# Kernel optimization log

Measured on AMD Instinct MI355X. Metric: run time of the kernel, lower is better.

The kernel has to match this reference:

```python
import jax, jax.numpy as jnp
import numpy as np

EPS = 1e-5
K = 20

def _bn(x, g, b, m, v, caxis):
    shape = [1] * x.ndim
    shape[caxis] = x.shape[caxis]
    rs = lambda p: p.reshape(shape)
    return (x - rs(m)) * (rs(g) / jnp.sqrt(rs(v) + EPS)) + rs(b)

def _lrelu(x):
    return jnp.where(x > 0, x, 0.2 * x)

def _graph_feature(x, k):
    # x: [B, C, N] -> [B, N, k, 2C]
    xt = jnp.swapaxes(x, 1, 2)                       # [B, N, C]
    xx = jnp.sum(x * x, axis=1)                      # [B, N]
    dist = xx[:, :, None] + xx[:, None, :] - 2.0 * jnp.einsum('bnc,bmc->bnm', xt, xt)
    _, idx = jax.lax.top_k(-dist, k)                 # smallest distances, [B, N, k]
    nbr = jax.vmap(lambda t, i: t[i])(xt, idx)       # [B, N, k, C]
    center = xt[:, :, None, :]
    return jnp.concatenate([jnp.broadcast_to(center, nbr.shape), nbr - center], axis=-1)

def _edgeconv(x, W, g, b, m, v, k):
    feat = _graph_feature(x, k)                      # [B, N, k, 2C]
    y = jnp.einsum('bnkc,oc->bonk', feat, W)         # 1x1 conv2d
    y = _lrelu(_bn(y, g, b, m, v, caxis=1))
    return jnp.max(y, axis=-1)                       # [B, O, N]


def setup_inputs() -> dict:
    key = jax.random.key(0)
    ks = jax.random.split(key, 40)
    d = {}
    d['x'] = jax.random.normal(ks[0], (8, 3, 2048), dtype=jnp.float32)
    def mk_w(k_, o, i):
        return jax.random.normal(k_, (o, i), dtype=jnp.float32) * (1.0 / np.sqrt(i))
    def mk_bn(k_, c, pfx, out):
        k1, k2, k3, k4 = jax.random.split(k_, 4)
        out[pfx + '_g'] = jax.random.normal(k1, (c,), jnp.float32) * 0.1 + 1.0
        out[pfx + '_b'] = jax.random.normal(k2, (c,), jnp.float32) * 0.1
        out[pfx + '_m'] = jax.random.normal(k3, (c,), jnp.float32) * 0.1
        out[pfx + '_v'] = jax.random.uniform(k4, (c,), jnp.float32) + 0.5
    d['W1'] = mk_w(ks[1], 64, 6);    mk_bn(ks[2], 64, 'bn1', d)
    d['W2'] = mk_w(ks[3], 64, 128);  mk_bn(ks[4], 64, 'bn2', d)
    d['W3'] = mk_w(ks[5], 128, 128); mk_bn(ks[6], 128, 'bn3', d)
    d['W4'] = mk_w(ks[7], 256, 256); mk_bn(ks[8], 256, 'bn4', d)
    d['W5'] = mk_w(ks[9], 1024, 512); mk_bn(ks[10], 1024, 'bn5', d)
    d['L1'] = mk_w(ks[11], 512, 2048); mk_bn(ks[12], 512, 'bn6', d)
    d['L2'] = mk_w(ks[13], 256, 512);  mk_bn(ks[14], 256, 'bn7', d)
    d['L3'] = mk_w(ks[15], 40, 256)
    d['L3_b'] = jax.random.normal(ks[16], (40,), jnp.float32) * 0.01
    return d


def reference(x, W1, bn1_g, bn1_b, bn1_m, bn1_v,
              W2, bn2_g, bn2_b, bn2_m, bn2_v,
              W3, bn3_g, bn3_b, bn3_m, bn3_v,
              W4, bn4_g, bn4_b, bn4_m, bn4_v,
              W5, bn5_g, bn5_b, bn5_m, bn5_v,
              L1, bn6_g, bn6_b, bn6_m, bn6_v,
              L2, bn7_g, bn7_b, bn7_m, bn7_v,
              L3, L3_b):
    x1 = _edgeconv(x,  W1, bn1_g, bn1_b, bn1_m, bn1_v, K)   # [B, 64, N]
    x2 = _edgeconv(x1, W2, bn2_g, bn2_b, bn2_m, bn2_v, K)   # [B, 64, N]
    x3 = _edgeconv(x2, W3, bn3_g, bn3_b, bn3_m, bn3_v, K)   # [B, 128, N]
    x4 = _edgeconv(x3, W4, bn4_g, bn4_b, bn4_m, bn4_v, K)   # [B, 256, N]
    xc = jnp.concatenate([x1, x2, x3, x4], axis=1)          # [B, 512, N]
    emb = _lrelu(_bn(jnp.einsum('bcn,oc->bon', xc, W5), bn5_g, bn5_b, bn5_m, bn5_v, caxis=1))
    feat = jnp.concatenate([jnp.max(emb, axis=-1), jnp.mean(emb, axis=-1)], axis=1)  # [B, 2048]
    h = _lrelu(_bn(feat @ L1.T, bn6_g, bn6_b, bn6_m, bn6_v, caxis=1))
    h = _lrelu(_bn(h @ L2.T, bn7_g, bn7_b, bn7_m, bn7_v, caxis=1))
    return h @ L3.T + L3_b
```

## Files before the change

### kernel.cpp

```cpp
#include <hip/hip_runtime.h>
#include <math.h>

#define NPTS 2048
#define KNN 20
#define EPS_BN 1e-5f

typedef unsigned short ushort;
typedef __attribute__((ext_vector_type(8))) short short8;
typedef __attribute__((ext_vector_type(4))) float float4v;

__device__ inline ushort bf16_rne(float x) {
    unsigned u = __float_as_uint(x);
    return (ushort)((u + 0x7fffu + ((u >> 16) & 1u)) >> 16);
}
__device__ inline float bf16_to_f(ushort h) {
    return __uint_as_float(((unsigned)h) << 16);
}
__device__ inline unsigned f32_sortable(float x) {
    unsigned u = __float_as_uint(x);
    return (u & 0x80000000u) ? ~u : (u | 0x80000000u);
}
__device__ inline float sortable_f32(unsigned s) {
    unsigned u = (s & 0x80000000u) ? (s ^ 0x80000000u) : ~s;
    return __uint_as_float(u);
}

__global__ __launch_bounds__(256) void xx_kernel(const float* __restrict__ xin,
                                                 long bstride,
                                                 float* __restrict__ xx, int C) {
    int b = blockIdx.y;
    int n = blockIdx.x * 256 + threadIdx.x;
    const float* xb = xin + (long)b * bstride;
    float s = 0.f;
    for (int c = 0; c < C; ++c) {
        float v = xb[(long)c * NPTS + n];
        s = fmaf(v, v, s);
    }
    xx[(long)b * NPTS + n] = s;
}

__global__ __launch_bounds__(512) void dist_topk_kernel(const float* __restrict__ xin,
                                                        long bstride,
                                                        const float* __restrict__ xx,
                                                        int* __restrict__ idxout, int C) {
    __shared__ float dist_s[8 * NPTS];
    int b = blockIdx.y;
    int n0 = blockIdx.x * 8;
    int tid = threadIdx.x;
    const float* xb = xin + (long)b * bstride;

    float acc[8][4];
#pragma unroll
    for (int r = 0; r < 8; ++r)
#pragma unroll
        for (int q = 0; q < 4; ++q) acc[r][q] = 0.f;

    for (int c = 0; c < C; ++c) {
        const float* row = xb + (long)c * NPTS;
        float4 xm4 = *(const float4*)(row + 4 * tid);
        float xm[4] = {xm4.x, xm4.y, xm4.z, xm4.w};
#pragma unroll
        for (int r = 0; r < 8; ++r) {
            float xnv = row[n0 + r];
#pragma unroll
            for (int q = 0; q < 4; ++q) acc[r][q] = fmaf(xnv, xm[q], acc[r][q]);
        }
    }

    const float* xxb = xx + (long)b * NPTS;
    float4 xxm4 = *(const float4*)(xxb + 4 * tid);
    float xxm[4] = {xxm4.x, xxm4.y, xxm4.z, xxm4.w};
    float xxn[8];
#pragma unroll
    for (int r = 0; r < 8; ++r) xxn[r] = xxb[n0 + r];

#pragma unroll
    for (int r = 0; r < 8; ++r) {
        float4 d;
        d.x = xxn[r] + xxm[0] - 2.f * acc[r][0];
        d.y = xxn[r] + xxm[1] - 2.f * acc[r][1];
        d.z = xxn[r] + xxm[2] - 2.f * acc[r][2];
        d.w = xxn[r] + xxm[3] - 2.f * acc[r][3];
        *(float4*)(dist_s + r * NPTS + 4 * tid) = d;
    }
    __syncthreads();

    int wave = tid >> 6, lane = tid & 63;
    int n = n0 + wave;
    float v[32];
#pragma unroll
    for (int i = 0; i < 32; ++i) v[i] = dist_s[wave * NPTS + lane + 64 * i];
    int* outp = idxout + ((long)b * NPTS + n) * KNN;

    float* wls = dist_s + wave * NPTS;

    float lm = v[0];
#pragma unroll
    for (int i = 1; i < 32; ++i) lm = fminf(lm, v[i]);
    unsigned sul = f32_sortable(lm);
    unsigned pmsk = 0, pval = 0;
    int need = 19;
#pragma unroll
    for (int bit = 31; bit >= 0; --bit) {
        unsigned bmv = 1u << bit;
        bool zero = ((sul & pmsk) == pval) && ((sul & bmv) == 0u);
        int cnt0 = (int)__popcll(__ballot(zero));
        if (need >= cnt0) { need -= cnt0; pval |= bmv; }
        pmsk |= bmv;
    }
    float T = sortable_f32(pval);

    float* cand_v = wls;
    int* cand_i = (int*)(wls + 64);
    int base = 0;
#pragma unroll
    for (int i = 0; i < 32; ++i) {
        bool pred = v[i] <= T;
        unsigned long long mask = __ballot(pred);
        int prefix = __builtin_amdgcn_mbcnt_hi(
            (unsigned)(mask >> 32),
            __builtin_amdgcn_mbcnt_lo((unsigned)mask, 0));
        if (pred) {
            int pos = base + prefix;
            if (pos < 64) { cand_v[pos] = v[i]; cand_i[pos] = lane + 64 * i; }
        }
        base += (int)__popcll(mask);
    }
    int M = base;

    if (M <= 64) {
        bool valid = lane < M;
        float cv = valid ? cand_v[lane] : 0.f;
        int ci = valid ? cand_i[lane] : 0;
        unsigned su2 = valid ? f32_sortable(cv) : 0xFFFFFFFFu;

        unsigned vpm = 0, vpv = 0;
        int vneed = 19;
#pragma unroll
        for (int bit = 31; bit >= 0; --bit) {
            unsigned bmv = 1u << bit;
            bool zero = ((su2 & vpm) == vpv) && ((su2 & bmv) == 0u);
            int cnt0 = (int)__popcll(__ballot(zero));
            if (vneed >= cnt0) { vneed -= cnt0; vpv |= bmv; }
            vpm |= bmv;
        }
        unsigned V = vpv;
        int cLess = (int)__popcll(__ballot(valid && su2 < V));
        bool tie = valid && (su2 == V);
        int e = (int)__popcll(__ballot(tie));
        int needT = 20 - cLess;
        bool win;
        if (needT >= e) {
            win = valid && (su2 <= V);
        } else {
            unsigned col = (unsigned)ci;
            unsigned cpm = 0, cpv = 0;
            int cneed = needT - 1;
#pragma unroll
            for (int bit = 10; bit >= 0; --bit) {
                unsigned bmv = 1u << bit;
                bool zero = tie && ((col & cpm) == cpv) && ((col & bmv) == 0u);
                int cnt0 = (int)__popcll(__ballot(zero));
                if (cneed >= cnt0) { cneed -= cnt0; cpv |= bmv; }
                cpm |= bmv;
            }
            win = valid && ((su2 < V) || (su2 == V && col <= cpv));
        }
        unsigned long long wm = __ballot(win);
        int prefix = __builtin_amdgcn_mbcnt_hi(
            (unsigned)(wm >> 32),
            __builtin_amdgcn_mbcnt_lo((unsigned)wm, 0));
        if (win) outp[prefix] = ci;
    } else {
        for (int kk = 0; kk < KNN; ++kk) {
            float bv = v[0];
            int bi = 0;
#pragma unroll
            for (int i = 1; i < 32; ++i)
                if (v[i] < bv) { bv = v[i]; bi = i; }
            int bm = lane + 64 * bi;
#pragma unroll
            for (int off = 32; off >= 1; off >>= 1) {
                float ov = __shfl_xor(bv, off, 64);
                int om = __shfl_xor(bm, off, 64);
                if (ov < bv || (ov == bv && om < bm)) { bv = ov; bm = om; }
            }
            if (lane == 0) outp[kk] = bm;
#pragma unroll
            for (int i = 0; i < 32; ++i)
                if (bm == lane + 64 * i) v[i] = 3.0e38f;
        }
    }
}

__global__ __launch_bounds__(256) void gemm_tu_kernel(
    const float* __restrict__ xin, long bstride, const float* __restrict__ W,
    const float* __restrict__ bg, const float* __restrict__ bb,
    const float* __restrict__ bm, const float* __restrict__ bv,
    float* __restrict__ tbuf, float* __restrict__ ubuf, int C, int O) {
    __shared__ float wa_s[128 * 16];
    __shared__ float wb_s[128 * 16];
    int b = blockIdx.z;
    int o0 = blockIdx.y * 16;
    int n0 = blockIdx.x * 256;
    int tid = threadIdx.x;

    for (int i = tid; i < C * 16; i += 256) {
        int c = i >> 4, ol = i & 15;
        float w1 = W[(long)(o0 + ol) * (2 * C) + c];
        float w2 = W[(long)(o0 + ol) * (2 * C) + C + c];
        wa_s[i] = w1 - w2;
        wb_s[i] = w2;
    }
    __syncthreads();

    float ta[16], ua[16];
#pragma unroll
    for (int ol = 0; ol < 16; ++ol) { ta[ol] = 0.f; ua[ol] = 0.f; }

    const float* xb = xin + (long)b * bstride;
    for (int c = 0; c < C; ++c) {
        float xv = xb[(long)c * NPTS + n0 + tid];
        const float* wac = wa_s + c * 16;
        const float* wbc = wb_s + c * 16;
#pragma unroll
        for (int ol = 0; ol < 16; ++ol) {
            ta[ol] = fmaf(wac[ol], xv, ta[ol]);
            ua[ol] = fmaf(wbc[ol], xv, ua[ol]);
        }
    }

#pragma unroll
    for (int ol = 0; ol < 16; ++ol) {
        int o = o0 + ol;
        float sc = bg[o] / sqrtf(bv[o] + EPS_BN);
        float bias = bb[o] - bm[o] * sc;
        long base = ((long)b * O + o) * NPTS + n0 + tid;
        tbuf[base] = ta[ol] * sc + bias;
        ubuf[base] = ua[ol] * sc;
    }
}

__global__ __launch_bounds__(256) void gather_kernel(const float* __restrict__ tbuf,
                                                     const float* __restrict__ ubuf,
                                                     const int* __restrict__ idx,
                                                     float* __restrict__ out, int O) {
    __shared__ float urow[NPTS];
    int o = blockIdx.x, half = blockIdx.y, b = blockIdx.z;
    int tid = threadIdx.x;
    const float4* up4 = (const float4*)(ubuf + ((long)b * O + o) * NPTS);
    float4* ur4 = (float4*)urow;
    for (int i = tid; i < NPTS / 4; i += 256) ur4[i] = up4[i];
    __syncthreads();

    const float* tp = tbuf + ((long)b * O + o) * NPTS;
    float* op = out + (long)b * (512 * NPTS) + (long)o * NPTS;
    int n = half * 1024 + tid * 4;
    float4 tv4 = *(const float4*)(tp + n);
    float tv[4] = {tv4.x, tv4.y, tv4.z, tv4.w};
    float res[4];
#pragma unroll
    for (int q = 0; q < 4; ++q) {
        const int4* ip = (const int4*)(idx + ((long)b * NPTS + n + q) * KNN);
        float mx = -3.0e38f;
#pragma unroll
        for (int jj = 0; jj < 5; ++jj) {
            int4 i4 = ip[jj];
            float y0 = tv[q] + urow[i4.x];
            float y1 = tv[q] + urow[i4.y];
            float y2 = tv[q] + urow[i4.z];
            float y3 = tv[q] + urow[i4.w];
            y0 = y0 > 0.f ? y0 : 0.2f * y0;
            y1 = y1 > 0.f ? y1 : 0.2f * y1;
            y2 = y2 > 0.f ? y2 : 0.2f * y2;
            y3 = y3 > 0.f ? y3 : 0.2f * y3;
            mx = fmaxf(mx, fmaxf(fmaxf(y0, y1), fmaxf(y2, y3)));
        }
        res[q] = mx;
    }
    *(float4*)(op + n) = make_float4(res[0], res[1], res[2], res[3]);
}

__global__ __launch_bounds__(256) void transpose_convert_kernel(
    const float* __restrict__ xc, ushort* __restrict__ xh, ushort* __restrict__ xl) {
    __shared__ float t[32 * 256];
    int c0 = blockIdx.x * 32, n0 = blockIdx.y * 256, b = blockIdx.z;
    int tid = threadIdx.x;
#pragma unroll
    for (int i = 0; i < 8; ++i) {
        int fi = i * 256 + tid;
        int c = fi >> 6, n4 = (fi & 63) * 4;
        *(float4*)(t + c * 256 + n4) =
            *(const float4*)(xc + ((long)b * 512 + c0 + c) * NPTS + n0 + n4);
    }
    __syncthreads();
    long obase = ((long)b * NPTS + n0 + tid) * 512 + c0;
#pragma unroll
    for (int g = 0; g < 8; ++g) {
        ushort h4[4], l4[4];
#pragma unroll
        for (int j = 0; j < 4; ++j) {
            float v = t[(g * 4 + j) * 256 + tid];
            ushort h = bf16_rne(v);
            h4[j] = h;
            l4[j] = bf16_rne(v - bf16_to_f(h));
        }
        *(ushort4*)(xh + obase + g * 4) = make_ushort4(h4[0], h4[1], h4[2], h4[3]);
        *(ushort4*)(xl + obase + g * 4) = make_ushort4(l4[0], l4[1], l4[2], l4[3]);
    }
}

__global__ __launch_bounds__(256) void w5_convert_kernel(const float* __restrict__ W5,
                                                         ushort* __restrict__ wh,
                                                         ushort* __restrict__ wl) {
    long i4 = ((long)blockIdx.x * 256 + threadIdx.x) * 4;
    float4 v = *(const float4*)(W5 + i4);
    float vv[4] = {v.x, v.y, v.z, v.w};
    ushort h4[4], l4[4];
#pragma unroll
    for (int j = 0; j < 4; ++j) {
        ushort h = bf16_rne(vv[j]);
        h4[j] = h;
        l4[j] = bf16_rne(vv[j] - bf16_to_f(h));
    }
    *(ushort4*)(wh + i4) = make_ushort4(h4[0], h4[1], h4[2], h4[3]);
    *(ushort4*)(wl + i4) = make_ushort4(l4[0], l4[1], l4[2], l4[3]);
}

__global__ __launch_bounds__(256) void prep_scb_kernel(const float* __restrict__ bg,
                                                       const float* __restrict__ bb,
                                                       const float* __restrict__ bm,
                                                       const float* __restrict__ bv,
                                                       float2* __restrict__ scb) {
    int o = blockIdx.x * 256 + threadIdx.x;
    float sc = bg[o] / sqrtf(bv[o] + EPS_BN);
    scb[o] = make_float2(sc, bb[o] - bm[o] * sc);
}

__global__ __launch_bounds__(256) void w5_mfma_kernel(
    const ushort* __restrict__ Wh, const ushort* __restrict__ Wl,
    const ushort* __restrict__ Xh, const ushort* __restrict__ Xl,
    const float2* __restrict__ scb, float* __restrict__ pmax,
    float* __restrict__ psum) {
    int b = blockIdx.z, nblk = blockIdx.y, oblk = blockIdx.x;
    int tid = threadIdx.x;
    int wave = tid >> 6, lane = tid & 63;
    int osub = wave & 1, nsub = wave >> 1;
    int o_base = oblk * 128 + osub * 64;
    int n_base = nblk * 128 + nsub * 64;
    int l15 = lane & 15, quad = lane >> 4;

    const ushort* Ah = Wh + (long)(o_base + l15) * 512 + quad * 8;
    const ushort* Al = Wl + (long)(o_base + l15) * 512 + quad * 8;
    const ushort* Bh = Xh + ((long)b * NPTS + n_base + l15) * 512 + quad * 8;
    const ushort* Bl = Xl + ((long)b * NPTS + n_base + l15) * 512 + quad * 8;

    float4v acc[4][4];
#pragma unroll
    for (int i = 0; i < 4; ++i)
#pragma unroll
        for (int j = 0; j < 4; ++j) acc[i][j] = (float4v)(0.f);

    for (int k = 0; k < 16; ++k) {
        int c0 = k * 32;
        short8 bh[4], bl[4];
#pragma unroll
        for (int tn = 0; tn < 4; ++tn) {
            bh[tn] = *(const short8*)(Bh + tn * (16 * 512) + c0);
            bl[tn] = *(const short8*)(Bl + tn * (16 * 512) + c0);
        }
#pragma unroll
        for (int to = 0; to < 4; ++to) {
            short8 ah = *(const short8*)(Ah + to * (16 * 512) + c0);
            short8 al = *(const short8*)(Al + to * (16 * 512) + c0);
#pragma unroll
            for (int tn = 0; tn < 4; ++tn) {
                acc[to][tn] =
                    __builtin_amdgcn_mfma_f32_16x16x32_bf16(ah, bh[tn], acc[to][tn], 0, 0, 0);
                acc[to][tn] =
                    __builtin_amdgcn_mfma_f32_16x16x32_bf16(ah, bl[tn], acc[to][tn], 0, 0, 0);
                acc[to][tn] =
                    __builtin_amdgcn_mfma_f32_16x16x32_bf16(al, bh[tn], acc[to][tn], 0, 0, 0);
            }
        }
    }

    int pidx = nblk * 2 + nsub;
#pragma unroll
    for (int to = 0; to < 4; ++to) {
        int ob = o_base + to * 16 + quad * 4;
        float mx[4], sm[4];
#pragma unroll
        for (int r = 0; r < 4; ++r) {
            float2 sb = scb[ob + r];
            float m = -3.0e38f, s = 0.f;
#pragma unroll
            for (int tn = 0; tn < 4; ++tn) {
                float y = acc[to][tn][r] * sb.x + sb.y;
                y = y > 0.f ? y : 0.2f * y;
                m = fmaxf(m, y);
                s += y;
            }
            mx[r] = m;
            sm[r] = s;
        }
#pragma unroll
        for (int r = 0; r < 4; ++r) {
#pragma unroll
            for (int off = 1; off < 16; off <<= 1) {
                mx[r] = fmaxf(mx[r], __shfl_xor(mx[r], off, 64));
                sm[r] += __shfl_xor(sm[r], off, 64);
            }
        }
        if (l15 == 0) {
            long base = ((long)pidx * 8 + b) * 1024 + ob;
#pragma unroll
            for (int r = 0; r < 4; ++r) {
                pmax[base + r] = mx[r];
                psum[base + r] = sm[r];
            }
        }
    }
}

__global__ __launch_bounds__(256) void w5_combine_kernel(const float* __restrict__ pmax,
                                                         const float* __restrict__ psum,
                                                         float* __restrict__ feat) {
    int b = blockIdx.x;
    for (int o = threadIdx.x; o < 1024; o += 256) {
        float m = -3.0e38f, s = 0.f;
        for (int p = 0; p < 32; ++p) {
            m = fmaxf(m, pmax[((long)p * 8 + b) * 1024 + o]);
            s += psum[((long)p * 8 + b) * 1024 + o];
        }
        feat[(long)b * 2048 + o] = m;
        feat[(long)b * 2048 + 1024 + o] = s * (1.f / 2048.f);
    }
}

__global__ __launch_bounds__(256) void fc_kernel(const float* __restrict__ in,
                                                 const float* __restrict__ W,
                                                 const float* __restrict__ bg,
                                                 const float* __restrict__ bb,
                                                 const float* __restrict__ bm,
                                                 const float* __restrict__ bv,
                                                 float* __restrict__ out, int I, int O,
                                                 int do_lrelu) {
    int b = blockIdx.y;
    int o = blockIdx.x * 4 + (threadIdx.x >> 6);
    int lane = threadIdx.x & 63;
    if (o < O) {
        const float* ip = in + (long)b * I;
        const float* wp = W + (long)o * I;
        float s = 0.f;
        for (int i = lane; i < I; i += 64) s = fmaf(ip[i], wp[i], s);
#pragma unroll
        for (int off = 32; off >= 1; off >>= 1) s += __shfl_xor(s, off, 64);
        if (lane == 0) {
            float y;
            if (bg) {
                float scv = bg[o] / sqrtf(bv[o] + EPS_BN);
                y = (s - bm[o]) * scv + bb[o];
                if (do_lrelu) y = y > 0.f ? y : 0.2f * y;
            } else {
                y = s + bb[o];
            }
            out[(long)b * O + o] = y;
        }
    }
}

extern "C" void kernel_launch(void* const* d_in, const int* in_sizes, int n_in,
                              void* d_out, int out_size, void* d_ws, size_t ws_size,
                              hipStream_t stream) {
    const float* x = (const float*)d_in[0];
    const float* W1 = (const float*)d_in[1];
    const float* W2 = (const float*)d_in[6];
    const float* W3 = (const float*)d_in[11];
    const float* W4 = (const float*)d_in[16];
    const float* W5 = (const float*)d_in[21];
    const float* L1 = (const float*)d_in[26];
    const float* L2 = (const float*)d_in[31];
    const float* L3 = (const float*)d_in[36];
    const float* L3b = (const float*)d_in[37];

    float* xc = (float*)d_ws;
    float* tb = xc + (long)8 * 512 * NPTS;
    float* ub = tb + (long)8 * 256 * NPTS;
    int* idx = (int*)(ub + (long)8 * 256 * NPTS);
    float* xxb = (float*)(idx + (long)8 * NPTS * KNN);
    float* feat = xxb + (long)8 * NPTS;
    float* h1 = feat + (long)8 * NPTS;
    float* h2 = h1 + (long)8 * 512;
    float* pmax = h2 + (long)8 * 256;
    float* psum = pmax + (long)32 * 8 * 1024;
    float2* scb = (float2*)(psum + (long)32 * 8 * 1024);
    ushort* W5h = (ushort*)(scb + 1024);
    ushort* W5l = W5h + (long)1024 * 512;
    ushort* Xh = (ushort*)tb;
    ushort* Xl = (ushort*)ub;

    struct Layer {
        const float* xin; long bstride; const float* W;
        const float *g, *b, *m, *v; int C, O, c0;
    };
    Layer layers[4] = {
        {x, (long)3 * NPTS, W1,
         (const float*)d_in[2], (const float*)d_in[3], (const float*)d_in[4], (const float*)d_in[5],
         3, 64, 0},
        {xc, (long)512 * NPTS, W2,
         (const float*)d_in[7], (const float*)d_in[8], (const float*)d_in[9], (const float*)d_in[10],
         64, 64, 64},
        {xc + (long)64 * NPTS, (long)512 * NPTS, W3,
         (const float*)d_in[12], (const float*)d_in[13], (const float*)d_in[14], (const float*)d_in[15],
         64, 128, 128},
        {xc + (long)128 * NPTS, (long)512 * NPTS, W4,
         (const float*)d_in[17], (const float*)d_in[18], (const float*)d_in[19], (const float*)d_in[20],
         128, 256, 256},
    };

    for (int l = 0; l < 4; ++l) {
        const Layer& L = layers[l];
        xx_kernel<<<dim3(NPTS / 256, 8), 256, 0, stream>>>(L.xin, L.bstride, xxb, L.C);
        dist_topk_kernel<<<dim3(NPTS / 8, 8), 512, 0, stream>>>(L.xin, L.bstride, xxb, idx, L.C);
        gemm_tu_kernel<<<dim3(NPTS / 256, L.O / 16, 8), 256, 0, stream>>>(
            L.xin, L.bstride, L.W, L.g, L.b, L.m, L.v, tb, ub, L.C, L.O);
        gather_kernel<<<dim3(L.O, 2, 8), 256, 0, stream>>>(tb, ub, idx, xc + (long)L.c0 * NPTS, L.O);
    }

    w5_convert_kernel<<<dim3(512), 256, 0, stream>>>(W5, W5h, W5l);
    prep_scb_kernel<<<dim3(4), 256, 0, stream>>>(
        (const float*)d_in[22], (const float*)d_in[23], (const float*)d_in[24],
        (const float*)d_in[25], scb);
    transpose_convert_kernel<<<dim3(16, 8, 8), 256, 0, stream>>>(xc, Xh, Xl);
    w5_mfma_kernel<<<dim3(8, 16, 8), 256, 0, stream>>>(W5h, W5l, Xh, Xl, scb, pmax, psum);
    w5_combine_kernel<<<dim3(8), 256, 0, stream>>>(pmax, psum, feat);

    fc_kernel<<<dim3(512 / 4, 8), 256, 0, stream>>>(
        feat, L1, (const float*)d_in[27], (const float*)d_in[28], (const float*)d_in[29],
        (const float*)d_in[30], h1, 2048, 512, 1);
    fc_kernel<<<dim3(256 / 4, 8), 256, 0, stream>>>(
        h1, L2, (const float*)d_in[32], (const float*)d_in[33], (const float*)d_in[34],
        (const float*)d_in[35], h2, 512, 256, 1);
    fc_kernel<<<dim3(10, 8), 256, 0, stream>>>(
        h2, L3, nullptr, L3b, nullptr, nullptr, (float*)d_out, 256, 40, 0);
}
```

Before: 957.5 us.

## Fuse squared-norm into distance/top-k kernel and process 16 rows per block

Removes the separate xx_kernel by computing each point's squared norm inside the distance loop, and takes the center-row norms from shared memory. The distance block grows to 1024 threads covering 16 query rows. The 16 rows are handled in two passes of 8 through the same shared buffer, and only 8 of the 16 waves run top-k in each pass. This saves a launch and halves how often the column data is reloaded per row, but it adds a serialized phase where half the waves sit idle and extra barriers.

```diff
diff --git a/kernel.cpp b/kernel.cpp
--- a/kernel.cpp
+++ b/kernel.cpp
@@ -25,170 +25,162 @@
     return __uint_as_float(u);
 }
 
-__global__ __launch_bounds__(256) void xx_kernel(const float* __restrict__ xin,
-                                                 long bstride,
-                                                 float* __restrict__ xx, int C) {
+__global__ __launch_bounds__(1024) void dist_topk_kernel(const float* __restrict__ xin,
+                                                         long bstride,
+                                                         int* __restrict__ idxout, int C) {
+    __shared__ float dist_s[8 * NPTS];
+    __shared__ float xxn_s[16];
     int b = blockIdx.y;
-    int n = blockIdx.x * 256 + threadIdx.x;
-    const float* xb = xin + (long)b * bstride;
-    float s = 0.f;
-    for (int c = 0; c < C; ++c) {
-        float v = xb[(long)c * NPTS + n];
-        s = fmaf(v, v, s);
-    }
-    xx[(long)b * NPTS + n] = s;
-}
-
-__global__ __launch_bounds__(512) void dist_topk_kernel(const float* __restrict__ xin,
-                                                        long bstride,
-                                                        const float* __restrict__ xx,
-                                                        int* __restrict__ idxout, int C) {
-    __shared__ float dist_s[8 * NPTS];
-    int b = blockIdx.y;
-    int n0 = blockIdx.x * 8;
+    int n0 = blockIdx.x * 16;
     int tid = threadIdx.x;
     const float* xb = xin + (long)b * bstride;
 
-    float acc[8][4];
-#pragma unroll
-    for (int r = 0; r < 8; ++r)
-#pragma unroll
-        for (int q = 0; q < 4; ++q) acc[r][q] = 0.f;
+    float acc[16][2];
+#pragma unroll
+    for (int r = 0; r < 16; ++r) { acc[r][0] = 0.f; acc[r][1] = 0.f; }
+    float xxm0 = 0.f, xxm1 = 0.f;
 
     for (int c = 0; c < C; ++c) {
         const float* row = xb + (long)c * NPTS;
-        float4 xm4 = *(const float4*)(row + 4 * tid);
-        float xm[4] = {xm4.x, xm4.y, xm4.z, xm4.w};
+        float2 xm2 = *(const float2*)(row + 2 * tid);
+        xxm0 = fmaf(xm2.x, xm2.x, xxm0);
+        xxm1 = fmaf(xm2.y, xm2.y, xxm1);
+#pragma unroll
+        for (int r = 0; r < 16; ++r) {
+            float xnv = row[n0 + r];
+            acc[r][0] = fmaf(xnv, xm2.x, acc[r][0]);
+            acc[r][1] = fmaf(xnv, xm2.y, acc[r][1]);
+        }
+    }
+
+    int diff = 2 * tid - n0;
+    if (diff >= 0 && diff < 16) {
+        xxn_s[diff] = xxm0;
+        xxn_s[diff + 1] = xxm1;
+    }
+    __syncthreads();
+
+    int wave = tid >> 6, lane = tid & 63;
+
+    for (int p = 0; p < 2; ++p) {
+        if (p) __syncthreads();
 #pragma unroll
         for (int r = 0; r < 8; ++r) {
-            float xnv = row[n0 + r];
-#pragma unroll
-            for (int q = 0; q < 4; ++q) acc[r][q] = fmaf(xnv, xm[q], acc[r][q]);
-        }
-    }
-
-    const float* xxb = xx + (long)b * NPTS;
-    float4 xxm4 = *(const float4*)(xxb + 4 * tid);
-    float xxm[4] = {xxm4.x, xxm4.y, xxm4.z, xxm4.w};
-    float xxn[8];
-#pragma unroll
-    for (int r = 0; r < 8; ++r) xxn[r] = xxb[n0 + r];
-
-#pragma unroll
-    for (int r = 0; r < 8; ++r) {
-        float4 d;
-        d.x = xxn[r] + xxm[0] - 2.f * acc[r][0];
-        d.y = xxn[r] + xxm[1] - 2.f * acc[r][1];
-        d.z = xxn[r] + xxm[2] - 2.f * acc[r][2];
-        d.w = xxn[r] + xxm[3] - 2.f * acc[r][3];
-        *(float4*)(dist_s + r * NPTS + 4 * tid) = d;
-    }
-    __syncthreads();
-
-    int wave = tid >> 6, lane = tid & 63;
-    int n = n0 + wave;
-    float v[32];
-#pragma unroll
-    for (int i = 0; i < 32; ++i) v[i] = dist_s[wave * NPTS + lane + 64 * i];
-    int* outp = idxout + ((long)b * NPTS + n) * KNN;
-
-    float* wls = dist_s + wave * NPTS;
-
-    float lm = v[0];
-#pragma unroll
-    for (int i = 1; i < 32; ++i) lm = fminf(lm, v[i]);
-    unsigned sul = f32_sortable(lm);
-    unsigned pmsk = 0, pval = 0;
-    int need = 19;
-#pragma unroll
-    for (int bit = 31; bit >= 0; --bit) {
-        unsigned bmv = 1u << bit;
-        bool zero = ((sul & pmsk) == pval) && ((sul & bmv) == 0u);
-        int cnt0 = (int)__popcll(__ballot(zero));
-        if (need >= cnt0) { need -= cnt0; pval |= bmv; }
-        pmsk |= bmv;
-    }
-    float T = sortable_f32(pval);
-
-    float* cand_v = wls;
-    int* cand_i = (int*)(wls + 64);
-    int base = 0;
-#pragma unroll
-    for (int i = 0; i < 32; ++i) {
-        bool pred = v[i] <= T;
-        unsigned long long mask = __ballot(pred);
-        int prefix = __builtin_amdgcn_mbcnt_hi(
-            (unsigned)(mask >> 32),
-            __builtin_amdgcn_mbcnt_lo((unsigned)mask, 0));
-        if (pred) {
-            int pos = base + prefix;
-            if (pos < 64) { cand_v[pos] = v[i]; cand_i[pos] = lane + 64 * i; }
-        }
-        base += (int)__popcll(mask);
-    }
-    int M = base;
-
-    if (M <= 64) {
-        bool valid = lane < M;
-        float cv = valid ? cand_v[lane] : 0.f;
-        int ci = valid ? cand_i[lane] : 0;
-        unsigned su2 = valid ? f32_sortable(cv) : 0xFFFFFFFFu;
-
-        unsigned vpm = 0, vpv = 0;
-        int vneed = 19;
-#pragma unroll
-        for (int bit = 31; bit >= 0; --bit) {
-            unsigned bmv = 1u << bit;
-            bool zero = ((su2 & vpm) == vpv) && ((su2 & bmv) == 0u);
-            int cnt0 = (int)__popcll(__ballot(zero));
-            if (vneed >= cnt0) { vneed -= cnt0; vpv |= bmv; }
-            vpm |= bmv;
-        }
-        unsigned V = vpv;
-        int cLess = (int)__popcll(__ballot(valid && su2 < V));
-        bool tie = valid && (su2 == V);
-        int e = (int)__popcll(__ballot(tie));
-        int needT = 20 - cLess;
-        bool win;
-        if (needT >= e) {
-            win = valid && (su2 <= V);
-        } else {
-            unsigned col = (unsigned)ci;
-            unsigned cpm = 0, cpv = 0;
-            int cneed = needT - 1;
-#pragma unroll
-            for (int bit = 10; bit >= 0; --bit) {
+            int rr = p * 8 + r;
+            float xxnr = xxn_s[rr];
+            float2 d;
+            d.x = xxnr + xxm0 - 2.f * acc[rr][0];
+            d.y = xxnr + xxm1 - 2.f * acc[rr][1];
+            *(float2*)(dist_s + r * NPTS + 2 * tid) = d;
+        }
+        __syncthreads();
+
+        if (wave < 8) {
+            int n = n0 + p * 8 + wave;
+            float v[32];
+#pragma unroll
+            for (int i = 0; i < 32; ++i) v[i] = dist_s[wave * NPTS + lane + 64 * i];
+            int* outp = idxout + ((long)b * NPTS + n) * KNN;
+
+            float* wls = dist_s + wave * NPTS;
+
+            float lm = v[0];
+#pragma unroll
+            for (int i = 1; i < 32; ++i) lm = fminf(lm, v[i]);
+            unsigned sul = f32_sortable(lm);
+            unsigned pmsk = 0, pval = 0;
+            int need = 19;
+#pragma unroll
+            for (int bit = 31; bit >= 0; --bit) {
                 unsigned bmv = 1u << bit;
-                bool zero = tie && ((col & cpm) == cpv) && ((col & bmv) == 0u);
+                bool zero = ((sul & pmsk) == pval) && ((sul & bmv) == 0u);
                 int cnt0 = (int)__popcll(__ballot(zero));
-                if (cneed >= cnt0) { cneed -= cnt0; cpv |= bmv; }
-                cpm |= bmv;
-            }
-            win = valid && ((su2 < V) || (su2 == V && col <= cpv));
-        }
-        unsigned long long wm = __ballot(win);
-        int prefix = __builtin_amdgcn_mbcnt_hi(
-            (unsigned)(wm >> 32),
-            __builtin_amdgcn_mbcnt_lo((unsigned)wm, 0));
-        if (win) outp[prefix] = ci;
-    } else {
-        for (int kk = 0; kk < KNN; ++kk) {
-            float bv = v[0];
-            int bi = 0;
-#pragma unroll
-            for (int i = 1; i < 32; ++i)
-                if (v[i] < bv) { bv = v[i]; bi = i; }
-            int bm = lane + 64 * bi;
-#pragma unroll
-            for (int off = 32; off >= 1; off >>= 1) {
-                float ov = __shfl_xor(bv, off, 64);
-                int om = __shfl_xor(bm, off, 64);
-                if (ov < bv || (ov == bv && om < bm)) { bv = ov; bm = om; }
-            }
-            if (lane == 0) outp[kk] = bm;
-#pragma unroll
-            for (int i = 0; i < 32; ++i)
-                if (bm == lane + 64 * i) v[i] = 3.0e38f;
+                if (need >= cnt0) { need -= cnt0; pval |= bmv; }
+                pmsk |= bmv;
+            }
+            float T = sortable_f32(pval);
+
+            float* cand_v = wls;
+            int* cand_i = (int*)(wls + 64);
+            int base = 0;
+#pragma unroll
+            for (int i = 0; i < 32; ++i) {
+                bool pred = v[i] <= T;
+                unsigned long long mask = __ballot(pred);
+                int prefix = __builtin_amdgcn_mbcnt_hi(
+                    (unsigned)(mask >> 32),
+                    __builtin_amdgcn_mbcnt_lo((unsigned)mask, 0));
+                if (pred) {
+                    int pos = base + prefix;
+                    if (pos < 64) { cand_v[pos] = v[i]; cand_i[pos] = lane + 64 * i; }
+                }
+                base += (int)__popcll(mask);
+            }
+            int M = base;
+
+            if (M <= 64) {
+                bool valid = lane < M;
+                float cv = valid ? cand_v[lane] : 0.f;
+                int ci = valid ? cand_i[lane] : 0;
+                unsigned su2 = valid ? f32_sortable(cv) : 0xFFFFFFFFu;
+
+                unsigned vpm = 0, vpv = 0;
+                int vneed = 19;
+#pragma unroll
+                for (int bit = 31; bit >= 0; --bit) {
+                    unsigned bmv = 1u << bit;
+                    bool zero = ((su2 & vpm) == vpv) && ((su2 & bmv) == 0u);
+                    int cnt0 = (int)__popcll(__ballot(zero));
+                    if (vneed >= cnt0) { vneed -= cnt0; vpv |= bmv; }
+                    vpm |= bmv;
+                }
+                unsigned V = vpv;
+                int cLess = (int)__popcll(__ballot(valid && su2 < V));
+                bool tie = valid && (su2 == V);
+                int e = (int)__popcll(__ballot(tie));
+                int needT = 20 - cLess;
+                bool win;
+                if (needT >= e) {
+                    win = valid && (su2 <= V);
+                } else {
+                    unsigned col = (unsigned)ci;
+                    unsigned cpm = 0, cpv = 0;
+                    int cneed = needT - 1;
+#pragma unroll
+                    for (int bit = 10; bit >= 0; --bit) {
+                        unsigned bmv = 1u << bit;
+                        bool zero = tie && ((col & cpm) == cpv) && ((col & bmv) == 0u);
+                        int cnt0 = (int)__popcll(__ballot(zero));
+                        if (cneed >= cnt0) { cneed -= cnt0; cpv |= bmv; }
+                        cpm |= bmv;
+                    }
+                    win = valid && ((su2 < V) || (su2 == V && col <= cpv));
+                }
+                unsigned long long wm = __ballot(win);
+                int prefix = __builtin_amdgcn_mbcnt_hi(
+                    (unsigned)(wm >> 32),
+                    __builtin_amdgcn_mbcnt_lo((unsigned)wm, 0));
+                if (win) outp[prefix] = ci;
+            } else {
+                for (int kk = 0; kk < KNN; ++kk) {
+                    float bv = v[0];
+                    int bi = 0;
+#pragma unroll
+                    for (int i = 1; i < 32; ++i)
+                        if (v[i] < bv) { bv = v[i]; bi = i; }
+                    int bm = lane + 64 * bi;
+#pragma unroll
+                    for (int off = 32; off >= 1; off >>= 1) {
+                        float ov = __shfl_xor(bv, off, 64);
+                        int om = __shfl_xor(bm, off, 64);
+                        if (ov < bv || (ov == bv && om < bm)) { bv = ov; bm = om; }
+                    }
+                    if (lane == 0) outp[kk] = bm;
+#pragma unroll
+                    for (int i = 0; i < 32; ++i)
+                        if (bm == lane + 64 * i) v[i] = 3.0e38f;
+                }
+            }
         }
     }
 }
@@ -521,8 +513,7 @@
 
     for (int l = 0; l < 4; ++l) {
         const Layer& L = layers[l];
-        xx_kernel<<<dim3(NPTS / 256, 8), 256, 0, stream>>>(L.xin, L.bstride, xxb, L.C);
-        dist_topk_kernel<<<dim3(NPTS / 8, 8), 512, 0, stream>>>(L.xin, L.bstride, xxb, idx, L.C);
+        dist_topk_kernel<<<dim3(NPTS / 16, 8), 1024, 0, stream>>>(L.xin, L.bstride, idx, L.C);
         gemm_tu_kernel<<<dim3(NPTS / 256, L.O / 16, 8), 256, 0, stream>>>(
             L.xin, L.bstride, L.W, L.g, L.b, L.m, L.v, tb, ub, L.C, L.O);
         gather_kernel<<<dim3(L.O, 2, 8), 256, 0, stream>>>(tb, ub, idx, xc + (long)L.c0 * NPTS, L.O);
```

New measurement: 1.152 ms. 1.2x slower.

## Halve kNN distance LDS buffer, stage query rows in LDS, prefetch next channel

Applied to the files above, without the earlier changes.

The distance/top-k kernel now stores only 4 distance rows at a time in shared memory (32KB instead of 64KB), processing the 8 query rows in two phases with half the waves selecting per phase. Query-point coordinates are staged once into shared memory and read as float4, and the next channel's candidate row is prefetched in a register. The smaller LDS footprint is meant to allow more resident blocks per CU, at the cost of an extra barrier and half the waves idling during each selection phase.

```diff
diff --git a/kernel.cpp b/kernel.cpp
--- a/kernel.cpp
+++ b/kernel.cpp
@@ -43,28 +43,37 @@
                                                         long bstride,
                                                         const float* __restrict__ xx,
                                                         int* __restrict__ idxout, int C) {
-    __shared__ float dist_s[8 * NPTS];
+    __shared__ float dist_s[4 * NPTS];
+    __shared__ float xn_s[128 * 8];
     int b = blockIdx.y;
     int n0 = blockIdx.x * 8;
     int tid = threadIdx.x;
     const float* xb = xin + (long)b * bstride;
 
+    for (int i = tid; i < C * 8; i += 512) {
+        int c = i >> 3, r = i & 7;
+        xn_s[i] = xb[(long)c * NPTS + n0 + r];
+    }
+    __syncthreads();
+
     float acc[8][4];
 #pragma unroll
     for (int r = 0; r < 8; ++r)
 #pragma unroll
         for (int q = 0; q < 4; ++q) acc[r][q] = 0.f;
 
+    float4 nxt = *(const float4*)(xb + 4 * tid);
     for (int c = 0; c < C; ++c) {
-        const float* row = xb + (long)c * NPTS;
-        float4 xm4 = *(const float4*)(row + 4 * tid);
+        float4 xm4 = nxt;
+        if (c + 1 < C) nxt = *(const float4*)(xb + (long)(c + 1) * NPTS + 4 * tid);
+        float4 a0 = *(const float4*)(xn_s + c * 8);
+        float4 a1 = *(const float4*)(xn_s + c * 8 + 4);
         float xm[4] = {xm4.x, xm4.y, xm4.z, xm4.w};
-#pragma unroll
-        for (int r = 0; r < 8; ++r) {
-            float xnv = row[n0 + r];
-#pragma unroll
-            for (int q = 0; q < 4; ++q) acc[r][q] = fmaf(xnv, xm[q], acc[r][q]);
-        }
+        float xn[8] = {a0.x, a0.y, a0.z, a0.w, a1.x, a1.y, a1.z, a1.w};
+#pragma unroll
+        for (int r = 0; r < 8; ++r)
+#pragma unroll
+            for (int q = 0; q < 4; ++q) acc[r][q] = fmaf(xn[r], xm[q], acc[r][q]);
     }
 
     const float* xxb = xx + (long)b * NPTS;
@@ -74,121 +83,129 @@
 #pragma unroll
     for (int r = 0; r < 8; ++r) xxn[r] = xxb[n0 + r];
 
-#pragma unroll
-    for (int r = 0; r < 8; ++r) {
-        float4 d;
-        d.x = xxn[r] + xxm[0] - 2.f * acc[r][0];
-        d.y = xxn[r] + xxm[1] - 2.f * acc[r][1];
-        d.z = xxn[r] + xxm[2] - 2.f * acc[r][2];
-        d.w = xxn[r] + xxm[3] - 2.f * acc[r][3];
-        *(float4*)(dist_s + r * NPTS + 4 * tid) = d;
-    }
-    __syncthreads();
-
     int wave = tid >> 6, lane = tid & 63;
-    int n = n0 + wave;
-    float v[32];
-#pragma unroll
-    for (int i = 0; i < 32; ++i) v[i] = dist_s[wave * NPTS + lane + 64 * i];
-    int* outp = idxout + ((long)b * NPTS + n) * KNN;
-
-    float* wls = dist_s + wave * NPTS;
-
-    float lm = v[0];
-#pragma unroll
-    for (int i = 1; i < 32; ++i) lm = fminf(lm, v[i]);
-    unsigned sul = f32_sortable(lm);
-    unsigned pmsk = 0, pval = 0;
-    int need = 19;
-#pragma unroll
-    for (int bit = 31; bit >= 0; --bit) {
-        unsigned bmv = 1u << bit;
-        bool zero = ((sul & pmsk) == pval) && ((sul & bmv) == 0u);
-        int cnt0 = (int)__popcll(__ballot(zero));
-        if (need >= cnt0) { need -= cnt0; pval |= bmv; }
-        pmsk |= bmv;
-    }
-    float T = sortable_f32(pval);
-
-    float* cand_v = wls;
-    int* cand_i = (int*)(wls + 64);
-    int base = 0;
-#pragma unroll
-    for (int i = 0; i < 32; ++i) {
-        bool pred = v[i] <= T;
-        unsigned long long mask = __ballot(pred);
-        int prefix = __builtin_amdgcn_mbcnt_hi(
-            (unsigned)(mask >> 32),
-            __builtin_amdgcn_mbcnt_lo((unsigned)mask, 0));
-        if (pred) {
-            int pos = base + prefix;
-            if (pos < 64) { cand_v[pos] = v[i]; cand_i[pos] = lane + 64 * i; }
-        }
-        base += (int)__popcll(mask);
-    }
-    int M = base;
-
-    if (M <= 64) {
-        bool valid = lane < M;
-        float cv = valid ? cand_v[lane] : 0.f;
-        int ci = valid ? cand_i[lane] : 0;
-        unsigned su2 = valid ? f32_sortable(cv) : 0xFFFFFFFFu;
-
-        unsigned vpm = 0, vpv = 0;
-        int vneed = 19;
-#pragma unroll
-        for (int bit = 31; bit >= 0; --bit) {
-            unsigned bmv = 1u << bit;
-            bool zero = ((su2 & vpm) == vpv) && ((su2 & bmv) == 0u);
-            int cnt0 = (int)__popcll(__ballot(zero));
-            if (vneed >= cnt0) { vneed -= cnt0; vpv |= bmv; }
-            vpm |= bmv;
-        }
-        unsigned V = vpv;
-        int cLess = (int)__popcll(__ballot(valid && su2 < V));
-        bool tie = valid && (su2 == V);
-        int e = (int)__popcll(__ballot(tie));
-        int needT = 20 - cLess;
-        bool win;
-        if (needT >= e) {
-            win = valid && (su2 <= V);
-        } else {
-            unsigned col = (unsigned)ci;
-            unsigned cpm = 0, cpv = 0;
-            int cneed = needT - 1;
-#pragma unroll
-            for (int bit = 10; bit >= 0; --bit) {
+    int rl = wave & 3;
+
+    for (int p = 0; p < 2; ++p) {
+        if (p) __syncthreads();
+#pragma unroll
+        for (int r = 0; r < 4; ++r) {
+            int rr = p * 4 + r;
+            float4 d;
+            d.x = xxn[rr] + xxm[0] - 2.f * acc[rr][0];
+            d.y = xxn[rr] + xxm[1] - 2.f * acc[rr][1];
+            d.z = xxn[rr] + xxm[2] - 2.f * acc[rr][2];
+            d.w = xxn[rr] + xxm[3] - 2.f * acc[rr][3];
+            *(float4*)(dist_s + r * NPTS + 4 * tid) = d;
+        }
+        __syncthreads();
+
+        if ((wave >> 2) == p) {
+            int n = n0 + p * 4 + rl;
+            float v[32];
+#pragma unroll
+            for (int i = 0; i < 32; ++i) v[i] = dist_s[rl * NPTS + lane + 64 * i];
+            int* outp = idxout + ((long)b * NPTS + n) * KNN;
+
+            float* wls = dist_s + rl * NPTS;
+
+            float lm = v[0];
+#pragma unroll
+            for (int i = 1; i < 32; ++i) lm = fminf(lm, v[i]);
+            unsigned sul = f32_sortable(lm);
+            unsigned pmsk = 0, pval = 0;
+            int need = 19;
+#pragma unroll
+            for (int bit = 31; bit >= 0; --bit) {
                 unsigned bmv = 1u << bit;
-                bool zero = tie && ((col & cpm) == cpv) && ((col & bmv) == 0u);
+                bool zero = ((sul & pmsk) == pval) && ((sul & bmv) == 0u);
                 int cnt0 = (int)__popcll(__ballot(zero));
-                if (cneed >= cnt0) { cneed -= cnt0; cpv |= bmv; }
-                cpm |= bmv;
-            }
-            win = valid && ((su2 < V) || (su2 == V && col <= cpv));
-        }
-        unsigned long long wm = __ballot(win);
-        int prefix = __builtin_amdgcn_mbcnt_hi(
-            (unsigned)(wm >> 32),
-            __builtin_amdgcn_mbcnt_lo((unsigned)wm, 0));
-        if (win) outp[prefix] = ci;
-    } else {
-        for (int kk = 0; kk < KNN; ++kk) {
-            float bv = v[0];
-            int bi = 0;
-#pragma unroll
-            for (int i = 1; i < 32; ++i)
-                if (v[i] < bv) { bv = v[i]; bi = i; }
-            int bm = lane + 64 * bi;
-#pragma unroll
-            for (int off = 32; off >= 1; off >>= 1) {
-                float ov = __shfl_xor(bv, off, 64);
-                int om = __shfl_xor(bm, off, 64);
-                if (ov < bv || (ov == bv && om < bm)) { bv = ov; bm = om; }
-            }
-            if (lane == 0) outp[kk] = bm;
-#pragma unroll
-            for (int i = 0; i < 32; ++i)
-                if (bm == lane + 64 * i) v[i] = 3.0e38f;
+                if (need >= cnt0) { need -= cnt0; pval |= bmv; }
+                pmsk |= bmv;
+            }
+            float T = sortable_f32(pval);
+
+            float* cand_v = wls;
+            int* cand_i = (int*)(wls + 64);
+            int base = 0;
+#pragma unroll
+            for (int i = 0; i < 32; ++i) {
+                bool pred = v[i] <= T;
+                unsigned long long mask = __ballot(pred);
+                int prefix = __builtin_amdgcn_mbcnt_hi(
+                    (unsigned)(mask >> 32),
+                    __builtin_amdgcn_mbcnt_lo((unsigned)mask, 0));
+                if (pred) {
+                    int pos = base + prefix;
+                    if (pos < 64) { cand_v[pos] = v[i]; cand_i[pos] = lane + 64 * i; }
+                }
+                base += (int)__popcll(mask);
+            }
+            int M = base;
+
+            if (M <= 64) {
+                bool valid = lane < M;
+                float cv = valid ? cand_v[lane] : 0.f;
+                int ci = valid ? cand_i[lane] : 0;
+                unsigned su2 = valid ? f32_sortable(cv) : 0xFFFFFFFFu;
+
+                unsigned vpm = 0, vpv = 0;
+                int vneed = 19;
+#pragma unroll
+                for (int bit = 31; bit >= 0; --bit) {
+                    unsigned bmv = 1u << bit;
+                    bool zero = ((su2 & vpm) == vpv) && ((su2 & bmv) == 0u);
+                    int cnt0 = (int)__popcll(__ballot(zero));
+                    if (vneed >= cnt0) { vneed -= cnt0; vpv |= bmv; }
+                    vpm |= bmv;
+                }
+                unsigned V = vpv;
+                int cLess = (int)__popcll(__ballot(valid && su2 < V));
+                bool tie = valid && (su2 == V);
+                int e = (int)__popcll(__ballot(tie));
+                int needT = 20 - cLess;
+                bool win;
+                if (needT >= e) {
+                    win = valid && (su2 <= V);
+                } else {
+                    unsigned col = (unsigned)ci;
+                    unsigned cpm = 0, cpv = 0;
+                    int cneed = needT - 1;
+#pragma unroll
+                    for (int bit = 10; bit >= 0; --bit) {
+                        unsigned bmv = 1u << bit;
+                        bool zero = tie && ((col & cpm) == cpv) && ((col & bmv) == 0u);
+                        int cnt0 = (int)__popcll(__ballot(zero));
+                        if (cneed >= cnt0) { cneed -= cnt0; cpv |= bmv; }
+                        cpm |= bmv;
+                    }
+                    win = valid && ((su2 < V) || (su2 == V && col <= cpv));
+                }
+                unsigned long long wm = __ballot(win);
+                int prefix = __builtin_amdgcn_mbcnt_hi(
+                    (unsigned)(wm >> 32),
+                    __builtin_amdgcn_mbcnt_lo((unsigned)wm, 0));
+                if (win) outp[prefix] = ci;
+            } else {
+                for (int kk = 0; kk < KNN; ++kk) {
+                    float bv = v[0];
+                    int bi = 0;
+#pragma unroll
+                    for (int i = 1; i < 32; ++i)
+                        if (v[i] < bv) { bv = v[i]; bi = i; }
+                    int bm = lane + 64 * bi;
+#pragma unroll
+                    for (int off = 32; off >= 1; off >>= 1) {
+                        float ov = __shfl_xor(bv, off, 64);
+                        int om = __shfl_xor(bm, off, 64);
+                        if (ov < bv || (ov == bv && om < bm)) { bv = ov; bm = om; }
+                    }
+                    if (lane == 0) outp[kk] = bm;
+#pragma unroll
+                    for (int i = 0; i < 32; ++i)
+                        if (bm == lane + 64 * i) v[i] = 3.0e38f;
+                }
+            }
         }
     }
 }
```

Measured after the change: 1.314 ms. 1.37x slower.

## Split fused distance/top-k kernel into chunked global-memory GEMM and selection kernels

Applied to the files above, without the earlier changes.

The fused distance+top-k kernel, which held a 64KB shared-memory distance tile per block, is split into a distance kernel that writes rows to a global scratch buffer in chunks of 512 rows and a separate selection kernel that reads them back with float4 loads. The selection kernel now needs only a small shared candidate buffer, so more blocks can be resident. Column indices are remapped to match the new vectorized load order, and the threshold comparison now uses sortable integers. The cost is an extra global round trip for the distance matrix and four times as many kernel launches per layer.

```diff
diff --git a/kernel.cpp b/kernel.cpp
--- a/kernel.cpp
+++ b/kernel.cpp
@@ -4,6 +4,7 @@
 #define NPTS 2048
 #define KNN 20
 #define EPS_BN 1e-5f
+#define RCHUNK 512
 
 typedef unsigned short ushort;
 typedef __attribute__((ext_vector_type(8))) short short8;
@@ -19,10 +20,6 @@
 __device__ inline unsigned f32_sortable(float x) {
     unsigned u = __float_as_uint(x);
     return (u & 0x80000000u) ? ~u : (u | 0x80000000u);
-}
-__device__ inline float sortable_f32(unsigned s) {
-    unsigned u = (s & 0x80000000u) ? (s ^ 0x80000000u) : ~s;
-    return __uint_as_float(u);
 }
 
 __global__ __launch_bounds__(256) void xx_kernel(const float* __restrict__ xin,
@@ -39,13 +36,13 @@
     xx[(long)b * NPTS + n] = s;
 }
 
-__global__ __launch_bounds__(512) void dist_topk_kernel(const float* __restrict__ xin,
+__global__ __launch_bounds__(512) void dist_gemm_kernel(const float* __restrict__ xin,
                                                         long bstride,
                                                         const float* __restrict__ xx,
-                                                        int* __restrict__ idxout, int C) {
-    __shared__ float dist_s[8 * NPTS];
+                                                        float* __restrict__ D,
+                                                        int C, int r0) {
     int b = blockIdx.y;
-    int n0 = blockIdx.x * 8;
+    int n0 = r0 + blockIdx.x * 8;
     int tid = threadIdx.x;
     const float* xb = xin + (long)b * bstride;
 
@@ -70,29 +67,41 @@
     const float* xxb = xx + (long)b * NPTS;
     float4 xxm4 = *(const float4*)(xxb + 4 * tid);
     float xxm[4] = {xxm4.x, xxm4.y, xxm4.z, xxm4.w};
-    float xxn[8];
-#pragma unroll
-    for (int r = 0; r < 8; ++r) xxn[r] = xxb[n0 + r];
 
 #pragma unroll
     for (int r = 0; r < 8; ++r) {
+        float xxn = xxb[n0 + r];
         float4 d;
-        d.x = xxn[r] + xxm[0] - 2.f * acc[r][0];
-        d.y = xxn[r] + xxm[1] - 2.f * acc[r][1];
-        d.z = xxn[r] + xxm[2] - 2.f * acc[r][2];
-        d.w = xxn[r] + xxm[3] - 2.f * acc[r][3];
-        *(float4*)(dist_s + r * NPTS + 4 * tid) = d;
-    }
-    __syncthreads();
-
+        d.x = xxn + xxm[0] - 2.f * acc[r][0];
+        d.y = xxn + xxm[1] - 2.f * acc[r][1];
+        d.z = xxn + xxm[2] - 2.f * acc[r][2];
+        d.w = xxn + xxm[3] - 2.f * acc[r][3];
+        long drow = ((long)b * RCHUNK + (n0 - r0) + r) * NPTS;
+        *(float4*)(D + drow + 4 * tid) = d;
+    }
+}
+
+__global__ __launch_bounds__(512) void topk_sel_kernel(const float* __restrict__ D,
+                                                       int* __restrict__ idxout, int r0) {
+    __shared__ float cvs[8][64];
+    __shared__ int cis[8][64];
+    int b = blockIdx.y;
+    int tid = threadIdx.x;
     int wave = tid >> 6, lane = tid & 63;
-    int n = n0 + wave;
+    int rloc = blockIdx.x * 8 + wave;
+    int n = r0 + rloc;
+    const float* Dp = D + ((long)b * RCHUNK + rloc) * NPTS;
+
     float v[32];
 #pragma unroll
-    for (int i = 0; i < 32; ++i) v[i] = dist_s[wave * NPTS + lane + 64 * i];
+    for (int j = 0; j < 8; ++j) {
+        float4 t = *(const float4*)(Dp + j * 256 + lane * 4);
+        v[j * 4 + 0] = t.x;
+        v[j * 4 + 1] = t.y;
+        v[j * 4 + 2] = t.z;
+        v[j * 4 + 3] = t.w;
+    }
     int* outp = idxout + ((long)b * NPTS + n) * KNN;
-
-    float* wls = dist_s + wave * NPTS;
 
     float lm = v[0];
 #pragma unroll
@@ -108,21 +117,24 @@
         if (need >= cnt0) { need -= cnt0; pval |= bmv; }
         pmsk |= bmv;
     }
-    float T = sortable_f32(pval);
-
-    float* cand_v = wls;
-    int* cand_i = (int*)(wls + 64);
+    unsigned Tsu = pval;
+
+    float* cand_v = cvs[wave];
+    int* cand_i = cis[wave];
     int base = 0;
 #pragma unroll
     for (int i = 0; i < 32; ++i) {
-        bool pred = v[i] <= T;
+        bool pred = f32_sortable(v[i]) <= Tsu;
         unsigned long long mask = __ballot(pred);
         int prefix = __builtin_amdgcn_mbcnt_hi(
             (unsigned)(mask >> 32),
             __builtin_amdgcn_mbcnt_lo((unsigned)mask, 0));
         if (pred) {
             int pos = base + prefix;
-            if (pos < 64) { cand_v[pos] = v[i]; cand_i[pos] = lane + 64 * i; }
+            if (pos < 64) {
+                cand_v[pos] = v[i];
+                cand_i[pos] = (i >> 2) * 256 + lane * 4 + (i & 3);
+            }
         }
         base += (int)__popcll(mask);
     }
@@ -178,17 +190,17 @@
 #pragma unroll
             for (int i = 1; i < 32; ++i)
                 if (v[i] < bv) { bv = v[i]; bi = i; }
-            int bm = lane + 64 * bi;
+            int bcol = (bi >> 2) * 256 + lane * 4 + (bi & 3);
 #pragma unroll
             for (int off = 32; off >= 1; off >>= 1) {
                 float ov = __shfl_xor(bv, off, 64);
-                int om = __shfl_xor(bm, off, 64);
-                if (ov < bv || (ov == bv && om < bm)) { bv = ov; bm = om; }
-            }
-            if (lane == 0) outp[kk] = bm;
+                int oc = __shfl_xor(bcol, off, 64);
+                if (ov < bv || (ov == bv && oc < bcol)) { bv = ov; bcol = oc; }
+            }
+            if (lane == 0) outp[kk] = bcol;
 #pragma unroll
             for (int i = 0; i < 32; ++i)
-                if (bm == lane + 64 * i) v[i] = 3.0e38f;
+                if (bcol == (i >> 2) * 256 + lane * 4 + (i & 3)) v[i] = 3.0e38f;
         }
     }
 }
@@ -497,6 +509,7 @@
     float2* scb = (float2*)(psum + (long)32 * 8 * 1024);
     ushort* W5h = (ushort*)(scb + 1024);
     ushort* W5l = W5h + (long)1024 * 512;
+    float* Dbuf = tb;
     ushort* Xh = (ushort*)tb;
     ushort* Xl = (ushort*)ub;
 
@@ -522,7 +535,11 @@
     for (int l = 0; l < 4; ++l) {
         const Layer& L = layers[l];
         xx_kernel<<<dim3(NPTS / 256, 8), 256, 0, stream>>>(L.xin, L.bstride, xxb, L.C);
-        dist_topk_kernel<<<dim3(NPTS / 8, 8), 512, 0, stream>>>(L.xin, L.bstride, xxb, idx, L.C);
+        for (int r0 = 0; r0 < NPTS; r0 += RCHUNK) {
+            dist_gemm_kernel<<<dim3(RCHUNK / 8, 8), 512, 0, stream>>>(
+                L.xin, L.bstride, xxb, Dbuf, L.C, r0);
+            topk_sel_kernel<<<dim3(RCHUNK / 8, 8), 512, 0, stream>>>(Dbuf, idx, r0);
+        }
         gemm_tu_kernel<<<dim3(NPTS / 256, L.O / 16, 8), 256, 0, stream>>>(
             L.xin, L.bstride, L.W, L.g, L.b, L.m, L.v, tb, ub, L.C, L.O);
         gather_kernel<<<dim3(L.O, 2, 8), 256, 0, stream>>>(tb, ub, idx, xc + (long)L.c0 * NPTS, L.O);
```

New measurement: 1.172 ms. +22.4%, slower.
